# Optimization experiments

Measured on AMD Instinct MI355X. Metric: run time of the kernel, lower is better.

The kernel has to match this reference:

```python
import jax, jax.numpy as jnp
import numpy as np

MAX_SENT_LEN = 28
B, LAT, D, E = 2048, 256, 1024, 256
LN_EPS = 1e-5


def setup_inputs() -> dict:
    key = jax.random.key(0)
    ks = jax.random.split(key, 10)
    s = 0.05
    return {
        "z": jax.random.normal(ks[0], (B, LAT), jnp.float32),
        "true_inp": jax.random.normal(ks[1], (B, MAX_SENT_LEN, E), jnp.float32),
        "tf_mask": jax.random.bernoulli(ks[2], 0.5, (MAX_SENT_LEN,)),
        "fc_w": jax.random.normal(ks[3], (D, LAT), jnp.float32) * s,
        "fc_b": jnp.zeros((D,), jnp.float32),
        "ln_w": jnp.ones((D,), jnp.float32),
        "ln_b": jnp.zeros((D,), jnp.float32),
        "w_ih": jax.random.normal(ks[4], (3 * D, D), jnp.float32) * s,
        "b_ih": jnp.zeros((3 * D,), jnp.float32),
        "w_hh": jax.random.normal(ks[5], (3 * D, D), jnp.float32) * s,
        "b_hh": jnp.zeros((3 * D,), jnp.float32),
    }


def reference(z, true_inp, tf_mask, fc_w, fc_b, ln_w, ln_b, w_ih, b_ih, w_hh, b_hh):
    # fc + layer norm -> initial hidden and (repeated) step input, [B, D]
    x = z @ fc_w.T + fc_b
    mu = jnp.mean(x, axis=-1, keepdims=True)
    var = jnp.mean(jnp.square(x - mu), axis=-1, keepdims=True)
    x = (x - mu) * jax.lax.rsqrt(var + LN_EPS) * ln_w + ln_b

    # encoded input is identical at every step -> precompute input gates once
    gi = x @ w_ih.T + b_ih                      # [B, 3D]
    i_r, i_z, i_n = jnp.split(gi, 3, axis=-1)

    # true_inp.repeat(1,1,repeating).transpose(1,0) -> [T, B, D]
    rep = D // E
    true_rep = jnp.transpose(jnp.tile(true_inp, (1, 1, rep)), (1, 0, 2))

    def step(h, inputs):
        t_inp, m = inputs
        h_in = jnp.where(m, t_inp, h)           # teacher-forcing branch
        gh = h_in @ w_hh.T + b_hh               # [B, 3D]
        h_r, h_z, h_n = jnp.split(gh, 3, axis=-1)
        r = jax.nn.sigmoid(i_r + h_r)
        u = jax.nn.sigmoid(i_z + h_z)
        n = jnp.tanh(i_n + r * h_n)
        h_new = (1.0 - u) * n + u * h_in
        return h_new, h_new

    _, outs = jax.lax.scan(step, x, (true_rep, tf_mask))
    return outs                                  # [T, B, D]
```

## Files before the change

### kernel.cpp

```cpp
#include <hip/hip_runtime.h>
#include <hip/hip_bf16.h>

#define TSTEPS 28

typedef __attribute__((ext_vector_type(8))) short bf16x8;
typedef __attribute__((ext_vector_type(4))) float f32x4;
typedef __attribute__((ext_vector_type(4))) unsigned short u16x4;
typedef __hip_bfloat16 bf16;

__device__ __forceinline__ unsigned short f2b(float f) {
  bf16 h = __float2bfloat16(f);
  return *reinterpret_cast<unsigned short*>(&h);
}
__device__ __forceinline__ float b2f(unsigned short u) {
  bf16 h = *reinterpret_cast<bf16*>(&u);
  return __bfloat162float(h);
}

__device__ __forceinline__ void gload16(const void* g, void* l) {
  __builtin_amdgcn_global_load_lds(
      (const __attribute__((address_space(1))) void*)g,
      (__attribute__((address_space(3))) void*)l, 16, 0, 0);
}

__device__ __forceinline__ float sigm(float x) { return 1.f / (1.f + __expf(-x)); }
__device__ __forceinline__ float tanh_fast(float x) {
  const float e2 = __expf(2.f * x);
  return 1.f - 2.f / (e2 + 1.f);
}

__device__ __forceinline__ bf16x8 cvt8(const float* src) {
  const float4 v0 = *(const float4*)src;
  const float4 v1 = *(const float4*)(src + 4);
  bf16x8 sv;
  sv[0] = (short)f2b(v0.x); sv[1] = (short)f2b(v0.y);
  sv[2] = (short)f2b(v0.z); sv[3] = (short)f2b(v0.w);
  sv[4] = (short)f2b(v1.x); sv[5] = (short)f2b(v1.y);
  sv[6] = (short)f2b(v1.z); sv[7] = (short)f2b(v1.w);
  return sv;
}

__global__ void conv_kernel(const float* __restrict__ in, unsigned short* __restrict__ out, int n4) {
  int i = blockIdx.x * blockDim.x + threadIdx.x;
  const int stride = gridDim.x * blockDim.x;
  for (; i < n4; i += stride) {
    const float4 v = *(const float4*)&in[(size_t)i * 4];
    u16x4 o;
    o.x = f2b(v.x); o.y = f2b(v.y); o.z = f2b(v.z); o.w = f2b(v.w);
    *(u16x4*)&out[(size_t)i * 4] = o;
  }
}

__global__ __launch_bounds__(256) void fold_kernel(const float* __restrict__ whh,
                                                   unsigned short* __restrict__ whf) {
  const int idx = blockIdx.x * 256 + threadIdx.x;
  const int n = idx >> 6, k4 = (idx & 63) << 2;
  const float* r = &whh[(size_t)n * 1024 + k4];
  const float4 a = *(const float4*)r;
  const float4 b = *(const float4*)(r + 256);
  const float4 c = *(const float4*)(r + 512);
  const float4 d = *(const float4*)(r + 768);
  u16x4 o;
  o.x = f2b(a.x + b.x + c.x + d.x);
  o.y = f2b(a.y + b.y + c.y + d.y);
  o.z = f2b(a.z + b.z + c.z + d.z);
  o.w = f2b(a.w + b.w + c.w + d.w);
  *(u16x4*)&whf[(size_t)n * 256 + k4] = o;
}

__global__ __launch_bounds__(256, 2) void gemm_fc_kernel(
    const float* __restrict__ A, const float* __restrict__ W,
    const float* __restrict__ bias, float* __restrict__ out) {
  constexpr int K = 256, NT = K / 32;
  __shared__ __align__(16) bf16 lds[2][6144];
  const int tid = threadIdx.x;
  const int lane = tid & 63;
  const int l15 = lane & 15, l4 = lane >> 4;
  const int wid = tid >> 6, wm = wid >> 1, wn = wid & 1;
  const int m0 = blockIdx.x * 128, n0 = blockIdx.y * 64;
  const int ra = tid >> 2, cb = (tid & 3) * 8;

  f32x4 acc[4][2] = {};

  auto STAGE = [&](int buf, int kt) {
    const int k0 = kt * 32;
    *(bf16x8*)&lds[buf][tid * 8]        = cvt8(&A[(size_t)(m0 + ra) * K + k0 + cb]);
    *(bf16x8*)&lds[buf][2048 + tid * 8] = cvt8(&A[(size_t)(m0 + 64 + ra) * K + k0 + cb]);
    *(bf16x8*)&lds[buf][4096 + tid * 8] = cvt8(&W[(size_t)(n0 + ra) * K + k0 + cb]);
  };

  STAGE(0, 0);
  __syncthreads();
  for (int kt = 0; kt < NT; ++kt) {
    const int buf = kt & 1;
    if (kt + 1 < NT) STAGE(buf ^ 1, kt + 1);
    bf16x8 af[4], bfr[2];
#pragma unroll
    for (int m = 0; m < 4; ++m)
      af[m] = *(const bf16x8*)&lds[buf][(wm * 64 + m * 16 + l15) * 32 + l4 * 8];
#pragma unroll
    for (int n = 0; n < 2; ++n)
      bfr[n] = *(const bf16x8*)&lds[buf][4096 + (wn * 32 + n * 16 + l15) * 32 + l4 * 8];
#pragma unroll
    for (int m = 0; m < 4; ++m)
#pragma unroll
      for (int n = 0; n < 2; ++n)
        acc[m][n] = __builtin_amdgcn_mfma_f32_16x16x32_bf16(af[m], bfr[n], acc[m][n], 0, 0, 0);
    __syncthreads();
  }

#pragma unroll
  for (int m = 0; m < 4; ++m) {
#pragma unroll
    for (int n = 0; n < 2; ++n) {
      const int col = n0 + wn * 32 + n * 16 + l15;
      const int rowb = m0 + wm * 64 + m * 16 + l4 * 4;
      const float bv = bias[col];
#pragma unroll
      for (int r = 0; r < 4; ++r)
        out[(size_t)(rowb + r) * 1024 + col] = acc[m][n][r] + bv;
    }
  }
}

__global__ __launch_bounds__(256) void ln_kernel(const float* __restrict__ x,
                                                 const float* __restrict__ w,
                                                 const float* __restrict__ b,
                                                 bf16* __restrict__ h0b,
                                                 float* __restrict__ h0f) {
  const int row = blockIdx.x, tid = threadIdx.x;
  const float4 v = *(const float4*)&x[(size_t)row * 1024 + tid * 4];
  float vv[4] = {v.x, v.y, v.z, v.w};
  float s = vv[0] + vv[1] + vv[2] + vv[3];
  float sq = vv[0] * vv[0] + vv[1] * vv[1] + vv[2] * vv[2] + vv[3] * vv[3];
#pragma unroll
  for (int off = 32; off; off >>= 1) {
    s += __shfl_down(s, off);
    sq += __shfl_down(sq, off);
  }
  __shared__ float sa[4], sb[4];
  const int lane = tid & 63, wid = tid >> 6;
  if (lane == 0) { sa[wid] = s; sb[wid] = sq; }
  __syncthreads();
  s = sa[0] + sa[1] + sa[2] + sa[3];
  sq = sb[0] + sb[1] + sb[2] + sb[3];
  const float mu = s * (1.f / 1024.f);
  const float var = sq * (1.f / 1024.f) - mu * mu;
  const float rs = rsqrtf(var + 1e-5f);
#pragma unroll
  for (int j = 0; j < 4; ++j) {
    const int c = tid * 4 + j;
    const float xv = (vv[j] - mu) * rs * w[c] + b[c];
    h0b[(size_t)row * 1024 + c] = __float2bfloat16(xv);
    h0f[(size_t)row * 1024 + c] = xv;
  }
}

__global__ __launch_bounds__(512, 4) void gemm_gi_kernel(
    const bf16* __restrict__ A,
    const float* __restrict__ W,
    const float* __restrict__ bias,
    unsigned short* __restrict__ out) {
  __shared__ __align__(16) bf16 lds[2][16384];
  const int tid = threadIdx.x;
  const int lane = tid & 63, l15 = lane & 15, l4 = lane >> 4;
  const int wid = tid >> 6, wm = wid >> 2, wn = wid & 3;
  const int n0 = blockIdx.x * 64, m0 = blockIdx.y * 64;

  f32x4 acc[3][2] = {};

  auto STAGE = [&](int buf, int kt) {
    const int k0 = kt * 64;
    {
      const int c = tid;
      const int row = c >> 3, kk = ((c & 7) ^ (row & 7)) * 8;
      gload16(&A[(size_t)(m0 + row) * 1024 + k0 + kk], &lds[buf][c * 8]);
    }
#pragma unroll
    for (int j = 0; j < 3; ++j) {
      const int c = tid + j * 512;
      const int row = c >> 3, kk = ((c & 7) ^ (row & 7)) * 8;
      *(bf16x8*)&lds[buf][4096 + c * 8] =
          cvt8(&W[(size_t)((row >> 6) * 1024 + n0 + (row & 63)) * 1024 + k0 + kk]);
    }
  };

  STAGE(0, 0);
  __syncthreads();
  for (int kt = 0; kt < 16; ++kt) {
    const int buf = kt & 1;
    if (kt + 1 < 16) STAGE(buf ^ 1, kt + 1);
#pragma unroll
    for (int ks = 0; ks < 2; ++ks) {
      const int x = (((ks << 2) | l4) ^ (l15 & 7)) * 8;
      bf16x8 af[2], bfr[3];
#pragma unroll
      for (int m = 0; m < 2; ++m)
        af[m] = *(const bf16x8*)&lds[buf][(wm * 32 + m * 16 + l15) * 64 + x];
#pragma unroll
      for (int g = 0; g < 3; ++g)
        bfr[g] = *(const bf16x8*)&lds[buf][4096 + (g * 64 + wn * 16 + l15) * 64 + x];
#pragma unroll
      for (int g = 0; g < 3; ++g)
#pragma unroll
        for (int m = 0; m < 2; ++m)
          acc[g][m] = __builtin_amdgcn_mfma_f32_16x16x32_bf16(af[m], bfr[g], acc[g][m], 0, 0, 0);
    }
    __syncthreads();
  }

  const int col = n0 + wn * 16 + l15;
#pragma unroll
  for (int g = 0; g < 3; ++g) {
    const float bv = bias[g * 1024 + col];
#pragma unroll
    for (int m = 0; m < 2; ++m) {
      const int rowb = m0 + wm * 32 + m * 16 + l4 * 4;
#pragma unroll
      for (int r = 0; r < 4; ++r)
        out[(size_t)(rowb + r) * 3072 + g * 1024 + col] = f2b(acc[g][m][r] + bv);
    }
  }
}

__global__ __launch_bounds__(512, 4) void batch_masked_kernel(
    const bf16* __restrict__ trueb,
    const int* __restrict__ tfmask,
    const bf16* __restrict__ whf,
    const float* __restrict__ bhh,
    const unsigned short* __restrict__ gib,
    float* __restrict__ out) {
  const int t = blockIdx.z;
  if (tfmask[t] == 0) return;
  __shared__ __align__(16) bf16 lds[2][16384];
  const int tid = threadIdx.x;
  const int lane = tid & 63, l15 = lane & 15, l4 = lane >> 4;
  const int wid = tid >> 6, wm = wid >> 2, wn = wid & 3;
  const int n0 = blockIdx.x * 64, m0 = blockIdx.y * 64;

  f32x4 acc[3][2] = {};

  auto STAGE = [&](int buf, int kt) {
    const int k0 = kt * 64;
    {
      const int c = tid;
      const int row = c >> 3, kk = ((c & 7) ^ (row & 7)) * 8;
      gload16(&trueb[((size_t)(m0 + row) * TSTEPS + t) * 256 + k0 + kk], &lds[buf][c * 8]);
    }
#pragma unroll
    for (int j = 0; j < 3; ++j) {
      const int c = tid + j * 512;
      const int row = c >> 3, kk = ((c & 7) ^ (row & 7)) * 8;
      gload16(&whf[(size_t)((row >> 6) * 1024 + n0 + (row & 63)) * 256 + k0 + kk],
              &lds[buf][4096 + c * 8]);
    }
  };

  STAGE(0, 0);
  __syncthreads();
  for (int kt = 0; kt < 4; ++kt) {
    const int buf = kt & 1;
    if (kt + 1 < 4) STAGE(buf ^ 1, kt + 1);
#pragma unroll
    for (int ks = 0; ks < 2; ++ks) {
      const int x = (((ks << 2) | l4) ^ (l15 & 7)) * 8;
      bf16x8 af[2], bfr[3];
#pragma unroll
      for (int m = 0; m < 2; ++m)
        af[m] = *(const bf16x8*)&lds[buf][(wm * 32 + m * 16 + l15) * 64 + x];
#pragma unroll
      for (int g = 0; g < 3; ++g)
        bfr[g] = *(const bf16x8*)&lds[buf][4096 + (g * 64 + wn * 16 + l15) * 64 + x];
#pragma unroll
      for (int g = 0; g < 3; ++g)
#pragma unroll
        for (int m = 0; m < 2; ++m)
          acc[g][m] = __builtin_amdgcn_mfma_f32_16x16x32_bf16(af[m], bfr[g], acc[g][m], 0, 0, 0);
    }
    __syncthreads();
  }

  float* outT = out + (size_t)t * 2048 * 1024;
  const int col = n0 + wn * 16 + l15;
  const float br = bhh[col], bz = bhh[col + 1024], bn_ = bhh[col + 2048];
  const unsigned short* tb = (const unsigned short*)trueb;
#pragma unroll
  for (int m = 0; m < 2; ++m) {
    const int rowb = m0 + wm * 32 + m * 16 + l4 * 4;
#pragma unroll
    for (int r = 0; r < 4; ++r) {
      const int row = rowb + r;
      const unsigned short* girow = &gib[(size_t)row * 3072];
      const float ir = b2f(girow[col]), iz = b2f(girow[col + 1024]), inn = b2f(girow[col + 2048]);
      const float hr = acc[0][m][r] + br;
      const float hz = acc[1][m][r] + bz;
      const float hn = acc[2][m][r] + bn_;
      const float hinv = b2f(tb[((size_t)row * TSTEPS + t) * 256 + (col & 255)]);
      const float rg = sigm(ir + hr);
      const float ug = sigm(iz + hz);
      const float ng = tanh_fast(inn + rg * hn);
      outT[(size_t)row * 1024 + col] = (1.f - ug) * ng + ug * hinv;
    }
  }
}

__global__ __launch_bounds__(512, 4) void step_kernel(
    const float* __restrict__ prevf,
    const bf16* __restrict__ hbfprev,
    bf16* __restrict__ hbfout,
    const int* __restrict__ tfmask,
    const bf16* __restrict__ whh,
    const float* __restrict__ bhh,
    const unsigned short* __restrict__ gib,
    float* __restrict__ out, int t) {
  if (tfmask[t] != 0) return;
  const bool predf32 = (t == 0) || (tfmask[t - 1] != 0);
  const int lid = blockIdx.x;
  const int xcd = lid & 7, rest = lid >> 3;
  const int m0 = (rest & 31) * 64;
  const int n0 = ((xcd << 1) | (rest >> 5)) * 64;

  __shared__ __align__(16) bf16 lds[2][16384];
  const int tid = threadIdx.x;
  const int lane = tid & 63, l15 = lane & 15, l4 = lane >> 4;
  const int wid = tid >> 6, wm = wid >> 2, wn = wid & 3;

  f32x4 acc[3][2] = {};

  auto STAGE = [&](int buf, int kt) {
    const int k0 = kt * 64;
    {
      const int c = tid;
      const int row = c >> 3, kk = ((c & 7) ^ (row & 7)) * 8;
      if (predf32) {
        *(bf16x8*)&lds[buf][c * 8] = cvt8(&prevf[(size_t)(m0 + row) * 1024 + k0 + kk]);
      } else {
        gload16(&hbfprev[(size_t)(m0 + row) * 1024 + k0 + kk], &lds[buf][c * 8]);
      }
    }
#pragma unroll
    for (int j = 0; j < 3; ++j) {
      const int c = tid + j * 512;
      const int row = c >> 3, kk = ((c & 7) ^ (row & 7)) * 8;
      gload16(&whh[(size_t)((row >> 6) * 1024 + n0 + (row & 63)) * 1024 + k0 + kk],
              &lds[buf][4096 + c * 8]);
    }
  };

  STAGE(0, 0);
  __syncthreads();
  for (int kt = 0; kt < 16; ++kt) {
    const int buf = kt & 1;
    if (kt + 1 < 16) STAGE(buf ^ 1, kt + 1);
#pragma unroll
    for (int ks = 0; ks < 2; ++ks) {
      const int x = (((ks << 2) | l4) ^ (l15 & 7)) * 8;
      bf16x8 af[2], bfr[3];
#pragma unroll
      for (int m = 0; m < 2; ++m)
        af[m] = *(const bf16x8*)&lds[buf][(wm * 32 + m * 16 + l15) * 64 + x];
#pragma unroll
      for (int g = 0; g < 3; ++g)
        bfr[g] = *(const bf16x8*)&lds[buf][4096 + (g * 64 + wn * 16 + l15) * 64 + x];
#pragma unroll
      for (int g = 0; g < 3; ++g)
#pragma unroll
        for (int m = 0; m < 2; ++m)
          acc[g][m] = __builtin_amdgcn_mfma_f32_16x16x32_bf16(af[m], bfr[g], acc[g][m], 0, 0, 0);
    }
    __syncthreads();
  }

  float* outT = out + (size_t)t * 2048 * 1024;
  const int col = n0 + wn * 16 + l15;
  const float br = bhh[col], bz = bhh[col + 1024], bn_ = bhh[col + 2048];
#pragma unroll
  for (int m = 0; m < 2; ++m) {
    const int rowb = m0 + wm * 32 + m * 16 + l4 * 4;
#pragma unroll
    for (int r = 0; r < 4; ++r) {
      const int row = rowb + r;
      const unsigned short* girow = &gib[(size_t)row * 3072];
      const float ir = b2f(girow[col]), iz = b2f(girow[col + 1024]), inn = b2f(girow[col + 2048]);
      const float hr = acc[0][m][r] + br;
      const float hz = acc[1][m][r] + bz;
      const float hn = acc[2][m][r] + bn_;
      const float hinv = prevf[(size_t)row * 1024 + col];
      const float rg = sigm(ir + hr);
      const float ug = sigm(iz + hz);
      const float ng = tanh_fast(inn + rg * hn);
      const float hnew = (1.f - ug) * ng + ug * hinv;
      outT[(size_t)row * 1024 + col] = hnew;
      hbfout[(size_t)row * 1024 + col] = __float2bfloat16(hnew);
    }
  }
}

extern "C" void kernel_launch(void* const* d_in, const int* in_sizes, int n_in,
                              void* d_out, int out_size, void* d_ws, size_t ws_size,
                              hipStream_t stream) {
  (void)in_sizes; (void)n_in; (void)out_size; (void)ws_size;
  const float* z = (const float*)d_in[0];
  const float* trueinp = (const float*)d_in[1];
  const int* tfmask = (const int*)d_in[2];
  const float* fc_w = (const float*)d_in[3];
  const float* fc_b = (const float*)d_in[4];
  const float* ln_w = (const float*)d_in[5];
  const float* ln_b = (const float*)d_in[6];
  const float* w_ih = (const float*)d_in[7];
  const float* b_ih = (const float*)d_in[8];
  const float* w_hh = (const float*)d_in[9];
  const float* b_hh = (const float*)d_in[10];
  float* out = (float*)d_out;

  char* ws = (char*)d_ws;
  size_t o = 0;
  float* xraw = (float*)(ws + o); o += (size_t)2048 * 1024 * 4;
  float* h0f  = (float*)(ws + o); o += (size_t)2048 * 1024 * 4;
  unsigned short* gib = (unsigned short*)(ws + o); o += (size_t)2048 * 3072 * 2;
  bf16* h0b   = (bf16*)(ws + o);  o += (size_t)2048 * 1024 * 2;
  bf16* hbf0  = (bf16*)(ws + o);  o += (size_t)2048 * 1024 * 2;
  bf16* hbf1  = (bf16*)(ws + o);  o += (size_t)2048 * 1024 * 2;
  bf16* whhb  = (bf16*)(ws + o);  o += (size_t)3072 * 1024 * 2;
  bf16* whf   = (bf16*)(ws + o);  o += (size_t)3072 * 256 * 2;
  bf16* trueb = (bf16*)(ws + o);  o += (size_t)2048 * TSTEPS * 256 * 2;

  conv_kernel<<<2048, 256, 0, stream>>>(w_hh, (unsigned short*)whhb, 3072 * 1024 / 4);
  conv_kernel<<<2048, 256, 0, stream>>>(trueinp, (unsigned short*)trueb, 2048 * TSTEPS * 256 / 4);
  fold_kernel<<<768, 256, 0, stream>>>(w_hh, (unsigned short*)whf);

  gemm_fc_kernel<<<dim3(16, 16), 256, 0, stream>>>(z, fc_w, fc_b, xraw);
  ln_kernel<<<2048, 256, 0, stream>>>(xraw, ln_w, ln_b, h0b, h0f);
  gemm_gi_kernel<<<dim3(16, 32), 512, 0, stream>>>(h0b, w_ih, b_ih, gib);

  batch_masked_kernel<<<dim3(16, 32, TSTEPS), 512, 0, stream>>>(trueb, tfmask, whf,
                                                                b_hh, gib, out);

  const float* prev = h0f;
  for (int t = 0; t < TSTEPS; ++t) {
    bf16* hw = (t & 1) ? hbf1 : hbf0;
    const bf16* hr = (t & 1) ? hbf0 : hbf1;
    step_kernel<<<512, 512, 0, stream>>>(prev, hr, hw, tfmask, whhb, b_hh, gib, out, t);
    prev = out + (size_t)t * 2048 * 1024;
  }
}
```

Before: 525.1 us.

## Store per-step bf16 hidden states and add 4-stage pipelined step kernel

Teacher-forced steps now also write a bf16 copy of their hidden state into a per-timestep workspace buffer. A new step kernel can then always read a bf16 previous hidden state instead of choosing between fp32 and bf16 inputs. The new kernel uses a 4-buffer global-to-LDS pipeline with K-tiles of 32 and explicit vmcnt waits, aiming to hide load latency in the recurrent GEMM. The w_hh bf16 conversion and the folding pass are merged into one kernel to save a read of the weights. The new path needs a large extra workspace and falls back to the old path if the workspace is too small.

```diff
diff --git a/kernel.cpp b/kernel.cpp
--- a/kernel.cpp
+++ b/kernel.cpp
@@ -51,8 +51,9 @@
   }
 }
 
-__global__ __launch_bounds__(256) void fold_kernel(const float* __restrict__ whh,
-                                                   unsigned short* __restrict__ whf) {
+__global__ __launch_bounds__(256) void convw_kernel(const float* __restrict__ whh,
+                                                    unsigned short* __restrict__ whhb,
+                                                    unsigned short* __restrict__ whf) {
   const int idx = blockIdx.x * 256 + threadIdx.x;
   const int n = idx >> 6, k4 = (idx & 63) << 2;
   const float* r = &whh[(size_t)n * 1024 + k4];
@@ -60,12 +61,21 @@
   const float4 b = *(const float4*)(r + 256);
   const float4 c = *(const float4*)(r + 512);
   const float4 d = *(const float4*)(r + 768);
-  u16x4 o;
-  o.x = f2b(a.x + b.x + c.x + d.x);
-  o.y = f2b(a.y + b.y + c.y + d.y);
-  o.z = f2b(a.z + b.z + c.z + d.z);
-  o.w = f2b(a.w + b.w + c.w + d.w);
-  *(u16x4*)&whf[(size_t)n * 256 + k4] = o;
+  u16x4 oa, ob, oc, od, of;
+  oa.x = f2b(a.x); oa.y = f2b(a.y); oa.z = f2b(a.z); oa.w = f2b(a.w);
+  ob.x = f2b(b.x); ob.y = f2b(b.y); ob.z = f2b(b.z); ob.w = f2b(b.w);
+  oc.x = f2b(c.x); oc.y = f2b(c.y); oc.z = f2b(c.z); oc.w = f2b(c.w);
+  od.x = f2b(d.x); od.y = f2b(d.y); od.z = f2b(d.z); od.w = f2b(d.w);
+  of.x = f2b(a.x + b.x + c.x + d.x);
+  of.y = f2b(a.y + b.y + c.y + d.y);
+  of.z = f2b(a.z + b.z + c.z + d.z);
+  of.w = f2b(a.w + b.w + c.w + d.w);
+  unsigned short* wb = &whhb[(size_t)n * 1024 + k4];
+  *(u16x4*)(wb)       = oa;
+  *(u16x4*)(wb + 256) = ob;
+  *(u16x4*)(wb + 512) = oc;
+  *(u16x4*)(wb + 768) = od;
+  *(u16x4*)&whf[(size_t)n * 256 + k4] = of;
 }
 
 __global__ __launch_bounds__(256, 2) void gemm_fc_kernel(
@@ -229,7 +239,8 @@
     const bf16* __restrict__ whf,
     const float* __restrict__ bhh,
     const unsigned short* __restrict__ gib,
-    float* __restrict__ out) {
+    float* __restrict__ out,
+    bf16* __restrict__ hbt) {
   const int t = blockIdx.z;
   if (tfmask[t] == 0) return;
   __shared__ __align__(16) bf16 lds[2][16384];
@@ -281,6 +292,7 @@
   }
 
   float* outT = out + (size_t)t * 2048 * 1024;
+  bf16* hbtT = hbt ? hbt + (size_t)t * 2048 * 1024 : nullptr;
   const int col = n0 + wn * 16 + l15;
   const float br = bhh[col], bz = bhh[col + 1024], bn_ = bhh[col + 2048];
   const unsigned short* tb = (const unsigned short*)trueb;
@@ -299,7 +311,109 @@
       const float rg = sigm(ir + hr);
       const float ug = sigm(iz + hz);
       const float ng = tanh_fast(inn + rg * hn);
-      outT[(size_t)row * 1024 + col] = (1.f - ug) * ng + ug * hinv;
+      const float hnew = (1.f - ug) * ng + ug * hinv;
+      outT[(size_t)row * 1024 + col] = hnew;
+      if (hbtT) hbtT[(size_t)row * 1024 + col] = __float2bfloat16(hnew);
+    }
+  }
+}
+
+__global__ __launch_bounds__(512, 2) void step2_kernel(
+    const bf16* __restrict__ prevb,
+    const float* __restrict__ prevf,
+    bf16* __restrict__ hbtout,
+    const int* __restrict__ tfmask,
+    const bf16* __restrict__ whh,
+    const float* __restrict__ bhh,
+    const unsigned short* __restrict__ gib,
+    float* __restrict__ out, int t) {
+  if (tfmask[t] != 0) return;
+  const int lid = blockIdx.x;
+  const int xcd = lid & 7, rest = lid >> 3;
+  const int m0 = (rest & 31) * 64;
+  const int n0 = ((xcd << 1) | (rest >> 5)) * 64;
+
+  __shared__ __align__(16) bf16 lds[4][8192];
+  const int tid = threadIdx.x;
+  const int lane = tid & 63, l15 = lane & 15, l4 = lane >> 4;
+  const int wid = tid >> 6, wm = wid >> 2, wn = wid & 3;
+
+  f32x4 acc[3][2] = {};
+
+  auto STAGE = [&](int buf, int kt) {
+    const int k0 = kt * 32;
+#pragma unroll
+    for (int j = 0; j < 2; ++j) {
+      const int c = tid + j * 512;
+      if (c < 256) {
+        const int row = c >> 2, kk = ((c & 3) ^ (row & 3)) * 8;
+        gload16(&prevb[(size_t)(m0 + row) * 1024 + k0 + kk], &lds[buf][c * 8]);
+      } else {
+        const int bc = c - 256;
+        const int row = bc >> 2, kk = ((bc & 3) ^ (row & 3)) * 8;
+        gload16(&whh[(size_t)((row >> 6) * 1024 + n0 + (row & 63)) * 1024 + k0 + kk],
+                &lds[buf][2048 + bc * 8]);
+      }
+    }
+  };
+
+  auto COMPUTE = [&](int buf) {
+    const int x = (l4 ^ (l15 & 3)) * 8;
+    bf16x8 af[2], bfr[3];
+#pragma unroll
+    for (int m = 0; m < 2; ++m)
+      af[m] = *(const bf16x8*)&lds[buf][(wm * 32 + m * 16 + l15) * 32 + x];
+#pragma unroll
+    for (int g = 0; g < 3; ++g)
+      bfr[g] = *(const bf16x8*)&lds[buf][2048 + (g * 64 + wn * 16 + l15) * 32 + x];
+#pragma unroll
+    for (int g = 0; g < 3; ++g)
+#pragma unroll
+      for (int m = 0; m < 2; ++m)
+        acc[g][m] = __builtin_amdgcn_mfma_f32_16x16x32_bf16(af[m], bfr[g], acc[g][m], 0, 0, 0);
+  };
+
+  STAGE(0, 0);
+  STAGE(1, 1);
+  STAGE(2, 2);
+  for (int kt = 0; kt < 30; ++kt) {
+    asm volatile("s_waitcnt vmcnt(4)" ::: "memory");
+    __builtin_amdgcn_s_barrier();
+    __builtin_amdgcn_sched_barrier(0);
+    COMPUTE(kt & 3);
+    __builtin_amdgcn_sched_barrier(0);
+    if (kt < 29) STAGE((kt + 3) & 3, kt + 3);
+  }
+  asm volatile("s_waitcnt vmcnt(2)" ::: "memory");
+  __builtin_amdgcn_s_barrier();
+  __builtin_amdgcn_sched_barrier(0);
+  COMPUTE(30 & 3);
+  asm volatile("s_waitcnt vmcnt(0)" ::: "memory");
+  __builtin_amdgcn_s_barrier();
+  __builtin_amdgcn_sched_barrier(0);
+  COMPUTE(31 & 3);
+
+  float* outT = out + (size_t)t * 2048 * 1024;
+  const int col = n0 + wn * 16 + l15;
+  const float br = bhh[col], bz = bhh[col + 1024], bn_ = bhh[col + 2048];
+#pragma unroll
+  for (int m = 0; m < 2; ++m) {
+    const int rowb = m0 + wm * 32 + m * 16 + l4 * 4;
+#pragma unroll
+    for (int r = 0; r < 4; ++r) {
+      const int row = rowb + r;
+      const unsigned short* girow = &gib[(size_t)row * 3072];
+      const float ir = b2f(girow[col]), iz = b2f(girow[col + 1024]), inn = b2f(girow[col + 2048]);
+      const float hr = acc[0][m][r] + br;
+      const float hz = acc[1][m][r] + bz;
+      const float hn = acc[2][m][r] + bn_;
+      const float hinv = prevf[(size_t)row * 1024 + col];
+      const float rg = sigm(ir + hr);
+      const float ug = sigm(iz + hz);
+      const float ng = tanh_fast(inn + rg * hn);
+      const float hnew = (1.f - ug) * ng + ug * hinv;
+      outT[(size_t)row * 1024 + col] = hnew;
+      hbtout[(size_t)row * 1024 + col] = __float2bfloat16(hnew);
     }
   }
 }
@@ -399,7 +513,7 @@
 extern "C" void kernel_launch(void* const* d_in, const int* in_sizes, int n_in,
                               void* d_out, int out_size, void* d_ws, size_t ws_size,
                               hipStream_t stream) {
-  (void)in_sizes; (void)n_in; (void)out_size; (void)ws_size;
+  (void)in_sizes; (void)n_in; (void)out_size;
   const float* z = (const float*)d_in[0];
   const float* trueinp = (const float*)d_in[1];
   const int* tfmask = (const int*)d_in[2];
@@ -424,23 +538,35 @@
   bf16* whhb  = (bf16*)(ws + o);  o += (size_t)3072 * 1024 * 2;
   bf16* whf   = (bf16*)(ws + o);  o += (size_t)3072 * 256 * 2;
   bf16* trueb = (bf16*)(ws + o);  o += (size_t)2048 * TSTEPS * 256 * 2;
-
-  conv_kernel<<<2048, 256, 0, stream>>>(w_hh, (unsigned short*)whhb, 3072 * 1024 / 4);
+  bf16* hbt   = (bf16*)(ws + o);
+  const size_t need_hbt = o + (size_t)TSTEPS * 2048 * 1024 * 2;
+  const bool use_hbt = (ws_size >= need_hbt);
+
+  convw_kernel<<<768, 256, 0, stream>>>(w_hh, (unsigned short*)whhb, (unsigned short*)whf);
   conv_kernel<<<2048, 256, 0, stream>>>(trueinp, (unsigned short*)trueb, 2048 * TSTEPS * 256 / 4);
-  fold_kernel<<<768, 256, 0, stream>>>(w_hh, (unsigned short*)whf);
 
   gemm_fc_kernel<<<dim3(16, 16), 256, 0, stream>>>(z, fc_w, fc_b, xraw);
   ln_kernel<<<2048, 256, 0, stream>>>(xraw, ln_w, ln_b, h0b, h0f);
   gemm_gi_kernel<<<dim3(16, 32), 512, 0, stream>>>(h0b, w_ih, b_ih, gib);
 
-  batch_masked_kernel<<<dim3(16, 32, TSTEPS), 512, 0, stream>>>(trueb, tfmask, whf,
-                                                                b_hh, gib, out);
-
-  const float* prev = h0f;
-  for (int t = 0; t < TSTEPS; ++t) {
-    bf16* hw = (t & 1) ? hbf1 : hbf0;
-    const bf16* hr = (t & 1) ? hbf0 : hbf1;
-    step_kernel<<<512, 512, 0, stream>>>(prev, hr, hw, tfmask, whhb, b_hh, gib, out, t);
-    prev = out + (size_t)t * 2048 * 1024;
-  }
-}
+  batch_masked_kernel<<<dim3(16, 32, TSTEPS), 512, 0, stream>>>(
+      trueb, tfmask, whf, b_hh, gib, out, use_hbt ? hbt : nullptr);
+
+  if (use_hbt) {
+    for (int t = 0; t < TSTEPS; ++t) {
+      const bf16* prevb = (t == 0) ? h0b : hbt + (size_t)(t - 1) * 2048 * 1024;
+      const float* prevf = (t == 0) ? h0f : out + (size_t)(t - 1) * 2048 * 1024;
+      bf16* hbtout = hbt + (size_t)t * 2048 * 1024;
+      step2_kernel<<<512, 512, 0, stream>>>(prevb, prevf, hbtout, tfmask, whhb, b_hh,
+                                            gib, out, t);
+    }
+  } else {
+    const float* prev = h0f;
+    for (int t = 0; t < TSTEPS; ++t) {
+      bf16* hw = (t & 1) ? hbf1 : hbf0;
+      const bf16* hr = (t & 1) ? hbf0 : hbf1;
+      step_kernel<<<512, 512, 0, stream>>>(prev, hr, hw, tfmask, whhb, b_hh, gib, out, t);
+      prev = out + (size_t)t * 2048 * 1024;
+    }
+  }
+}
```

Result: slower. 591.5 us (+12.6%).

## Pair teacher-forced timesteps per block and fuse weight conversion kernels

Applied to the files above, without the earlier changes.

The batched teacher-forced kernel now handles two timesteps per block, loading the folded W_hh tile once and reusing it for both timesteps' MFMA accumulations, which halves weight traffic and block count for that stage. The separate bf16 conversion of W_hh and its fold kernel are merged into one kernel that reads w_hh once and writes both outputs. In exchange, the paired kernel uses more LDS and registers, so its launch bound drops to 2 blocks per CU, which may cut occupancy.

```diff
diff --git a/kernel.cpp b/kernel.cpp
--- a/kernel.cpp
+++ b/kernel.cpp
@@ -51,8 +51,9 @@
   }
 }
 
-__global__ __launch_bounds__(256) void fold_kernel(const float* __restrict__ whh,
-                                                   unsigned short* __restrict__ whf) {
+__global__ __launch_bounds__(256) void convw_kernel(const float* __restrict__ whh,
+                                                    unsigned short* __restrict__ whhb,
+                                                    unsigned short* __restrict__ whf) {
   const int idx = blockIdx.x * 256 + threadIdx.x;
   const int n = idx >> 6, k4 = (idx & 63) << 2;
   const float* r = &whh[(size_t)n * 1024 + k4];
@@ -60,12 +61,21 @@
   const float4 b = *(const float4*)(r + 256);
   const float4 c = *(const float4*)(r + 512);
   const float4 d = *(const float4*)(r + 768);
-  u16x4 o;
-  o.x = f2b(a.x + b.x + c.x + d.x);
-  o.y = f2b(a.y + b.y + c.y + d.y);
-  o.z = f2b(a.z + b.z + c.z + d.z);
-  o.w = f2b(a.w + b.w + c.w + d.w);
-  *(u16x4*)&whf[(size_t)n * 256 + k4] = o;
+  u16x4 oa, ob, oc, od, of;
+  oa.x = f2b(a.x); oa.y = f2b(a.y); oa.z = f2b(a.z); oa.w = f2b(a.w);
+  ob.x = f2b(b.x); ob.y = f2b(b.y); ob.z = f2b(b.z); ob.w = f2b(b.w);
+  oc.x = f2b(c.x); oc.y = f2b(c.y); oc.z = f2b(c.z); oc.w = f2b(c.w);
+  od.x = f2b(d.x); od.y = f2b(d.y); od.z = f2b(d.z); od.w = f2b(d.w);
+  of.x = f2b(a.x + b.x + c.x + d.x);
+  of.y = f2b(a.y + b.y + c.y + d.y);
+  of.z = f2b(a.z + b.z + c.z + d.z);
+  of.w = f2b(a.w + b.w + c.w + d.w);
+  unsigned short* wb = &whhb[(size_t)n * 1024 + k4];
+  *(u16x4*)(wb)       = oa;
+  *(u16x4*)(wb + 256) = ob;
+  *(u16x4*)(wb + 512) = oc;
+  *(u16x4*)(wb + 768) = od;
+  *(u16x4*)&whf[(size_t)n * 256 + k4] = of;
 }
 
 __global__ __launch_bounds__(256, 2) void gemm_fc_kernel(
@@ -223,36 +233,43 @@
   }
 }
 
-__global__ __launch_bounds__(512, 4) void batch_masked_kernel(
+__global__ __launch_bounds__(512, 2) void batch_pair_kernel(
     const bf16* __restrict__ trueb,
     const int* __restrict__ tfmask,
     const bf16* __restrict__ whf,
     const float* __restrict__ bhh,
     const unsigned short* __restrict__ gib,
     float* __restrict__ out) {
-  const int t = blockIdx.z;
-  if (tfmask[t] == 0) return;
-  __shared__ __align__(16) bf16 lds[2][16384];
+  const int p = blockIdx.z;
+  const int t1 = 2 * p, t2 = 2 * p + 1;
+  const bool m1 = tfmask[t1] != 0;
+  const bool m2 = tfmask[t2] != 0;
+  if (!m1 && !m2) return;
+  __shared__ __align__(16) bf16 lds[2][20480];
   const int tid = threadIdx.x;
   const int lane = tid & 63, l15 = lane & 15, l4 = lane >> 4;
   const int wid = tid >> 6, wm = wid >> 2, wn = wid & 3;
   const int n0 = blockIdx.x * 64, m0 = blockIdx.y * 64;
 
-  f32x4 acc[3][2] = {};
+  f32x4 acc1[3][2] = {}, acc2[3][2] = {};
 
   auto STAGE = [&](int buf, int kt) {
     const int k0 = kt * 64;
     {
       const int c = tid;
       const int row = c >> 3, kk = ((c & 7) ^ (row & 7)) * 8;
-      gload16(&trueb[((size_t)(m0 + row) * TSTEPS + t) * 256 + k0 + kk], &lds[buf][c * 8]);
+      if (m1)
+        gload16(&trueb[((size_t)(m0 + row) * TSTEPS + t1) * 256 + k0 + kk], &lds[buf][c * 8]);
+      if (m2)
+        gload16(&trueb[((size_t)(m0 + row) * TSTEPS + t2) * 256 + k0 + kk],
+                &lds[buf][4096 + c * 8]);
     }
 #pragma unroll
     for (int j = 0; j < 3; ++j) {
       const int c = tid + j * 512;
       const int row = c >> 3, kk = ((c & 7) ^ (row & 7)) * 8;
       gload16(&whf[(size_t)((row >> 6) * 1024 + n0 + (row & 63)) * 256 + k0 + kk],
-              &lds[buf][4096 + c * 8]);
+              &lds[buf][8192 + c * 8]);
     }
   };
 
@@ -264,44 +281,63 @@
 #pragma unroll
     for (int ks = 0; ks < 2; ++ks) {
       const int x = (((ks << 2) | l4) ^ (l15 & 7)) * 8;
-      bf16x8 af[2], bfr[3];
-#pragma unroll
-      for (int m = 0; m < 2; ++m)
-        af[m] = *(const bf16x8*)&lds[buf][(wm * 32 + m * 16 + l15) * 64 + x];
+      bf16x8 bfr[3];
 #pragma unroll
       for (int g = 0; g < 3; ++g)
-        bfr[g] = *(const bf16x8*)&lds[buf][4096 + (g * 64 + wn * 16 + l15) * 64 + x];
-#pragma unroll
-      for (int g = 0; g < 3; ++g)
+        bfr[g] = *(const bf16x8*)&lds[buf][8192 + (g * 64 + wn * 16 + l15) * 64 + x];
+      if (m1) {
+        bf16x8 af[2];
 #pragma unroll
         for (int m = 0; m < 2; ++m)
-          acc[g][m] = __builtin_amdgcn_mfma_f32_16x16x32_bf16(af[m], bfr[g], acc[g][m], 0, 0, 0);
+          af[m] = *(const bf16x8*)&lds[buf][(wm * 32 + m * 16 + l15) * 64 + x];
+#pragma unroll
+        for (int g = 0; g < 3; ++g)
+#pragma unroll
+          for (int m = 0; m < 2; ++m)
+            acc1[g][m] = __builtin_amdgcn_mfma_f32_16x16x32_bf16(af[m], bfr[g], acc1[g][m], 0, 0, 0);
+      }
+      if (m2) {
+        bf16x8 af[2];
+#pragma unroll
+        for (int m = 0; m < 2; ++m)
+          af[m] = *(const bf16x8*)&lds[buf][4096 + (wm * 32 + m * 16 + l15) * 64 + x];
+#pragma unroll
+        for (int g = 0; g < 3; ++g)
+#pragma unroll
+          for (int m = 0; m < 2; ++m)
+            acc2[g][m] = __builtin_amdgcn_mfma_f32_16x16x32_bf16(af[m], bfr[g], acc2[g][m], 0, 0, 0);
+      }
     }
     __syncthreads();
   }
 
-  float* outT = out + (size_t)t * 2048 * 1024;
   const int col = n0 + wn * 16 + l15;
   const float br = bhh[col], bz = bhh[col + 1024], bn_ = bhh[col + 2048];
   const unsigned short* tb = (const unsigned short*)trueb;
-#pragma unroll
-  for (int m = 0; m < 2; ++m) {
-    const int rowb = m0 + wm * 32 + m * 16 + l4 * 4;
-#pragma unroll
-    for (int r = 0; r < 4; ++r) {
-      const int row = rowb + r;
-      const unsigned short* girow = &gib[(size_t)row * 3072];
-      const float ir = b2f(girow[col]), iz = b2f(girow[col + 1024]), inn = b2f(girow[col + 2048]);
-      const float hr = acc[0][m][r] + br;
-      const float hz = acc[1][m][r] + bz;
-      const float hn = acc[2][m][r] + bn_;
-      const float hinv = b2f(tb[((size_t)row * TSTEPS + t) * 256 + (col & 255)]);
-      const float rg = sigm(ir + hr);
-      const float ug = sigm(iz + hz);
-      const float ng = tanh_fast(inn + rg * hn);
-      outT[(size_t)row * 1024 + col] = (1.f - ug) * ng + ug * hinv;
-    }
-  }
+
+  auto EPI = [&](int t, f32x4 (&acc)[3][2]) {
+    float* outT = out + (size_t)t * 2048 * 1024;
+#pragma unroll
+    for (int m = 0; m < 2; ++m) {
+      const int rowb = m0 + wm * 32 + m * 16 + l4 * 4;
+#pragma unroll
+      for (int r = 0; r < 4; ++r) {
+        const int row = rowb + r;
+        const unsigned short* girow = &gib[(size_t)row * 3072];
+        const float ir = b2f(girow[col]), iz = b2f(girow[col + 1024]), inn = b2f(girow[col + 2048]);
+        const float hr = acc[0][m][r] + br;
+        const float hz = acc[1][m][r] + bz;
+        const float hn = acc[2][m][r] + bn_;
+        const float hinv = b2f(tb[((size_t)row * TSTEPS + t) * 256 + (col & 255)]);
+        const float rg = sigm(ir + hr);
+        const float ug = sigm(iz + hz);
+        const float ng = tanh_fast(inn + rg * hn);
+        outT[(size_t)row * 1024 + col] = (1.f - ug) * ng + ug * hinv;
+      }
+    }
+  };
+  if (m1) EPI(t1, acc1);
+  if (m2) EPI(t2, acc2);
 }
 
 __global__ __launch_bounds__(512, 4) void step_kernel(
@@ -425,16 +461,15 @@
   bf16* whf   = (bf16*)(ws + o);  o += (size_t)3072 * 256 * 2;
   bf16* trueb = (bf16*)(ws + o);  o += (size_t)2048 * TSTEPS * 256 * 2;
 
-  conv_kernel<<<2048, 256, 0, stream>>>(w_hh, (unsigned short*)whhb, 3072 * 1024 / 4);
+  convw_kernel<<<768, 256, 0, stream>>>(w_hh, (unsigned short*)whhb, (unsigned short*)whf);
   conv_kernel<<<2048, 256, 0, stream>>>(trueinp, (unsigned short*)trueb, 2048 * TSTEPS * 256 / 4);
-  fold_kernel<<<768, 256, 0, stream>>>(w_hh, (unsigned short*)whf);
 
   gemm_fc_kernel<<<dim3(16, 16), 256, 0, stream>>>(z, fc_w, fc_b, xraw);
   ln_kernel<<<2048, 256, 0, stream>>>(xraw, ln_w, ln_b, h0b, h0f);
   gemm_gi_kernel<<<dim3(16, 32), 512, 0, stream>>>(h0b, w_ih, b_ih, gib);
 
-  batch_masked_kernel<<<dim3(16, 32, TSTEPS), 512, 0, stream>>>(trueb, tfmask, whf,
-                                                                b_hh, gib, out);
+  batch_pair_kernel<<<dim3(16, 32, TSTEPS / 2), 512, 0, stream>>>(trueb, tfmask, whf,
+                                                                  b_hh, gib, out);
 
   const float* prev = h0f;
   for (int t = 0; t < TSTEPS; ++t) {
```

Result: faster. 512.4 us (-2.4%).
